# Optimization experiments

Measured on AMD Instinct MI355X. Metric: run time of the kernel, lower is better.

Reference implementation:

```python
import jax, jax.numpy as jnp
import numpy as np

NUM_LAYERS = 2
# Z eigenvalue of each basis state index (bit0 = qubit 0 = MSB, bit1 = qubit 1)
_Z0 = jnp.array([1.0, 1.0, -1.0, -1.0], dtype=jnp.float32)
_Z1 = jnp.array([1.0, -1.0, 1.0, -1.0], dtype=jnp.float32)
_CNOT_PERM = jnp.array([0, 1, 3, 2])  # CNOT(control=0, target=1) permutes |10>,|11>


def setup_inputs() -> dict:
    key = jax.random.key(0)
    k1, k2 = jax.random.split(key)
    x = jax.random.uniform(k1, (8192, 56, 56), dtype=jnp.float32)
    params = jax.random.uniform(k2, (2,), dtype=jnp.float32)
    return {"x": x, "params": params}


def reference(x, params):
    # x: (N, H, W). Each 2x2 patch contributes its top-row pair (x[r,c], x[r,c+1]).
    p0 = x[:, ::2, ::2]   # (N, H//2, W//2) -> angle for qubit 0
    p1 = x[:, ::2, 1::2]  # (N, H//2, W//2) -> angle for qubit 1
    # torch: patch.max() is the max over the whole (N, 2) slice at each (r, c)
    m = jnp.maximum(p0, p1).max(axis=0)  # (H//2, W//2)
    t0 = jnp.pi * p0 / (m + 1e-8)
    t1 = jnp.pi * p1 / (m + 1e-8)

    # RY(t)|0> = cos(t/2)|0> + sin(t/2)|1>; product state amplitudes, index = 2*b0 + b1
    c0, s0 = jnp.cos(t0 * 0.5), jnp.sin(t0 * 0.5)
    c1, s1 = jnp.cos(t1 * 0.5), jnp.sin(t1 * 0.5)
    a = jnp.stack([c0 * c1, c0 * s1, s0 * c1, s0 * s1], axis=-1).astype(jnp.complex64)

    # RZ(p) = diag(e^{-ip/2}, e^{+ip/2}) on each qubit -> diagonal phase per basis state
    phase = jnp.exp(-0.5j * (params[0] * _Z0 + params[1] * _Z1)).astype(jnp.complex64)
    for _ in range(NUM_LAYERS):
        a = a * phase          # RZ(params[0]) on q0, RZ(params[1]) on q1
        a = a[..., _CNOT_PERM]  # CNOT(0 -> 1)

    probs = jnp.real(a * jnp.conj(a))           # (N, H//2, W//2, 4)
    z0 = jnp.einsum('nhwk,k->nhw', probs, _Z0)  # <Z_0> (analytic expectation)
    N = x.shape[0]
    return z0.reshape(N, -1)  # (N, (H//2)*(W//2)), row-major matches r-then-c loop
```

## Files before the change

### kernel.cpp

```cpp
#include <hip/hip_runtime.h>


namespace {

constexpr int IMG  = 56 * 56;
constexpr int HW   = 28 * 28;
constexpr int NIMG = 8192;
constexpr int NB1  = 512;
constexpr int IPB  = NIMG / NB1;

__global__ __launch_bounds__(256) void k_partial(const float* __restrict__ x,
                                                 float* __restrict__ M,
                                                 unsigned* __restrict__ mu) {
    const int t = threadIdx.x;
    const int b = blockIdx.x;

    int   hw[4];
    int   off[4];
    float lm[4];
#pragma unroll
    for (int s = 0; s < 4; ++s) {
        hw[s] = t + s * 256;
        if (hw[s] < HW) {
            int h  = hw[s] / 28;
            int w  = hw[s] - h * 28;
            off[s] = h * 112 + w * 2;
        } else {
            off[s] = -1;
        }
        lm[s] = 0.0f;
    }

    if (b == 0) {
#pragma unroll
        for (int s = 0; s < 4; ++s)
            if (off[s] >= 0) mu[hw[s]] = 0u;
    }

    const float* base = x + (size_t)b * IPB * IMG;
#pragma unroll
    for (int n = 0; n < IPB; ++n) {
#pragma unroll
        for (int s = 0; s < 4; ++s) {
            if (off[s] >= 0) {
                float2 v = *(const float2*)(base + (size_t)n * IMG + off[s]);
                lm[s] = fmaxf(lm[s], fmaxf(v.x, v.y));
            }
        }
    }

#pragma unroll
    for (int s = 0; s < 4; ++s)
        if (off[s] >= 0) M[b * HW + hw[s]] = lm[s];
}

__global__ __launch_bounds__(256) void k_final(const float* __restrict__ M,
                                               unsigned* __restrict__ mu) {
    int u = blockIdx.x * 256 + threadIdx.x;
    if (u >= HW * 16) return;
    int g   = u / HW;
    int col = u - g * HW;
    float cm = 0.0f;
#pragma unroll
    for (int k = 0; k < 32; ++k)
        cm = fmaxf(cm, M[(g * 32 + k) * HW + col]);
    atomicMax(mu + col, __float_as_uint(cm));
}

__global__ __launch_bounds__(256) void k_out(const float* __restrict__ x,
                                             const float* __restrict__ m,
                                             float* __restrict__ out) {
    int g  = blockIdx.x * 256 + threadIdx.x;
    int n  = g / 392;
    int j  = g - n * 392;
    int h  = j / 14;
    int w2 = j - h * 14;

    float4 v  = *(const float4*)(x + (size_t)n * IMG + h * 112 + w2 * 4);
    float2 mm = *(const float2*)(m + h * 28 + w2 * 2);

    float2 o;
    o.x = __builtin_amdgcn_cosf(v.x * (0.5f / (mm.x + 1e-8f)));
    o.y = __builtin_amdgcn_cosf(v.z * (0.5f / (mm.y + 1e-8f)));

    *(float2*)(out + (size_t)n * HW + h * 28 + w2 * 2) = o;
}

}

extern "C" void kernel_launch(void* const* d_in, const int* in_sizes, int n_in,
                              void* d_out, int out_size, void* d_ws, size_t ws_size,
                              hipStream_t stream) {
    const float* x   = (const float*)d_in[0];
    float*       M   = (float*)d_ws;
    unsigned*    mu  = (unsigned*)((char*)d_ws + (size_t)NB1 * HW * 4);
    float*       out = (float*)d_out;

    hipLaunchKernelGGL(k_partial, dim3(NB1), dim3(256), 0, stream, x, M, mu);
    hipLaunchKernelGGL(k_final, dim3((HW * 16 + 255) / 256), dim3(256), 0, stream,
                       M, mu);
    hipLaunchKernelGGL(k_out, dim3(NIMG * 392 / 256), dim3(256), 0, stream,
                       x, (const float*)mu, out);
}
```

Measured before the change: 45.70 us.

## Widen loads to float4 in reduction and output kernels, double partial-max blocks

```diff
diff --git a/kernel.cpp b/kernel.cpp
--- a/kernel.cpp
+++ b/kernel.cpp
@@ -3,11 +3,12 @@
 
 namespace {
 
-constexpr int IMG  = 56 * 56;
-constexpr int HW   = 28 * 28;
+constexpr int IMG  = 3136;
+constexpr int HW   = 784;
 constexpr int NIMG = 8192;
-constexpr int NB1  = 512;
+constexpr int NB1  = 1024;
 constexpr int IPB  = NIMG / NB1;
+constexpr int NQ   = 392;
 
 __global__ __launch_bounds__(256) void k_partial(const float* __restrict__ x,
                                                  float* __restrict__ M,
@@ -15,75 +16,75 @@
     const int t = threadIdx.x;
     const int b = blockIdx.x;
 
-    int   hw[4];
-    int   off[4];
-    float lm[4];
-#pragma unroll
-    for (int s = 0; s < 4; ++s) {
-        hw[s] = t + s * 256;
-        if (hw[s] < HW) {
-            int h  = hw[s] / 28;
-            int w  = hw[s] - h * 28;
-            off[s] = h * 112 + w * 2;
-        } else {
-            off[s] = -1;
-        }
-        lm[s] = 0.0f;
+    if (b == 0) {
+        for (int i = t; i < HW; i += 256) mu[i] = 0u;
     }
 
-    if (b == 0) {
-#pragma unroll
-        for (int s = 0; s < 4; ++s)
-            if (off[s] >= 0) mu[hw[s]] = 0u;
-    }
+    const int h0 = t / 14,   w0 = t - h0 * 14;
+    const int o0 = h0 * 112 + w0 * 4;
+    const int u1 = t + 256;
+    const int h1 = u1 / 14,  w1 = u1 - h1 * 14;
+    const int o1 = h1 * 112 + w1 * 4;
+    const bool a1 = (u1 < NQ);
+
+    float2 lm0 = make_float2(0.f, 0.f);
+    float2 lm1 = make_float2(0.f, 0.f);
 
     const float* base = x + (size_t)b * IPB * IMG;
 #pragma unroll
     for (int n = 0; n < IPB; ++n) {
-#pragma unroll
-        for (int s = 0; s < 4; ++s) {
-            if (off[s] >= 0) {
-                float2 v = *(const float2*)(base + (size_t)n * IMG + off[s]);
-                lm[s] = fmaxf(lm[s], fmaxf(v.x, v.y));
-            }
+        const float* p = base + (size_t)n * IMG;
+        float4 v = *(const float4*)(p + o0);
+        lm0.x = fmaxf(lm0.x, fmaxf(v.x, v.y));
+        lm0.y = fmaxf(lm0.y, fmaxf(v.z, v.w));
+        if (a1) {
+            float4 w = *(const float4*)(p + o1);
+            lm1.x = fmaxf(lm1.x, fmaxf(w.x, w.y));
+            lm1.y = fmaxf(lm1.y, fmaxf(w.z, w.w));
         }
     }
 
-#pragma unroll
-    for (int s = 0; s < 4; ++s)
-        if (off[s] >= 0) M[b * HW + hw[s]] = lm[s];
+    *(float2*)(M + (size_t)b * HW + 2 * t) = lm0;
+    if (a1) *(float2*)(M + (size_t)b * HW + 2 * u1) = lm1;
 }
 
 __global__ __launch_bounds__(256) void k_final(const float* __restrict__ M,
                                                unsigned* __restrict__ mu) {
     int u = blockIdx.x * 256 + threadIdx.x;
-    if (u >= HW * 16) return;
     int g   = u / HW;
     int col = u - g * HW;
+    const float* p = M + (size_t)g * 32 * HW + col;
     float cm = 0.0f;
 #pragma unroll
     for (int k = 0; k < 32; ++k)
-        cm = fmaxf(cm, M[(g * 32 + k) * HW + col]);
+        cm = fmaxf(cm, p[k * HW]);
     atomicMax(mu + col, __float_as_uint(cm));
 }
 
 __global__ __launch_bounds__(256) void k_out(const float* __restrict__ x,
-                                             const float* __restrict__ m,
+                                             const float* __restrict__ mu,
                                              float* __restrict__ out) {
     int g  = blockIdx.x * 256 + threadIdx.x;
-    int n  = g / 392;
-    int j  = g - n * 392;
-    int h  = j / 14;
-    int w2 = j - h * 14;
+    int n  = g / 196;
+    int j  = g - n * 196;
+    int h  = j / 7;
+    int wq = j - h * 7;
 
-    float4 v  = *(const float4*)(x + (size_t)n * IMG + h * 112 + w2 * 4);
-    float2 mm = *(const float2*)(m + h * 28 + w2 * 2);
+    const float* p = x + (size_t)n * IMG + h * 112 + 8 * wq;
+    float4 va = *(const float4*)p;
+    float4 vb = *(const float4*)(p + 4);
 
-    float2 o;
-    o.x = __builtin_amdgcn_cosf(v.x * (0.5f / (mm.x + 1e-8f)));
-    o.y = __builtin_amdgcn_cosf(v.z * (0.5f / (mm.y + 1e-8f)));
+    const float* mp = mu + h * 28 + 4 * wq;
+    float2 ma = *(const float2*)mp;
+    float2 mb = *(const float2*)(mp + 2);
 
-    *(float2*)(out + (size_t)n * HW + h * 28 + w2 * 2) = o;
+    float4 o;
+    o.x = __builtin_amdgcn_cosf(va.x * (0.5f / (ma.x + 1e-8f)));
+    o.y = __builtin_amdgcn_cosf(va.z * (0.5f / (ma.y + 1e-8f)));
+    o.z = __builtin_amdgcn_cosf(vb.x * (0.5f / (mb.x + 1e-8f)));
+    o.w = __builtin_amdgcn_cosf(vb.z * (0.5f / (mb.y + 1e-8f)));
+
+    *(float4*)(out + (size_t)n * HW + 4 * j) = o;
 }
 
 }
@@ -97,8 +98,7 @@
     float*       out = (float*)d_out;
 
     hipLaunchKernelGGL(k_partial, dim3(NB1), dim3(256), 0, stream, x, M, mu);
-    hipLaunchKernelGGL(k_final, dim3((HW * 16 + 255) / 256), dim3(256), 0, stream,
-                       M, mu);
-    hipLaunchKernelGGL(k_out, dim3(NIMG * 392 / 256), dim3(256), 0, stream,
+    hipLaunchKernelGGL(k_final, dim3(HW * 32 / 256), dim3(256), 0, stream, M, mu);
+    hipLaunchKernelGGL(k_out, dim3(NIMG * 196 / 256), dim3(256), 0, stream,
                        x, (const float*)mu, out);
 }
```

New measurement: 36.74 us. 19.6% less time.
